# Optimization experiments

Measured on AMD Instinct MI355X. Metric: run time of the kernel, lower is better.

## Reference

```python
import jax, jax.numpy as jnp
import numpy as np

B = 8192
INPUT_DIM = 1024
PATH_DIM = 256
HIDDEN_DIM = 1024
OUTPUT_DIM = 1024
STEPS = 50


def setup_inputs() -> dict:
    key = jax.random.key(0)
    ks = jax.random.split(key, 12)
    s = lambda fan_in: 1.0 / np.sqrt(fan_in)
    x0 = jax.random.normal(ks[0], (B, INPUT_DIM), dtype=jnp.float32)
    W_pe = jax.random.uniform(ks[1], (INPUT_DIM, PATH_DIM), jnp.float32, -s(INPUT_DIM), s(INPUT_DIM))
    b_pe = jax.random.uniform(ks[2], (PATH_DIM,), jnp.float32, -s(INPUT_DIM), s(INPUT_DIM))
    W_hi = jax.random.uniform(ks[3], (INPUT_DIM, HIDDEN_DIM), jnp.float32, -s(INPUT_DIM), s(INPUT_DIM))
    b_hi = jax.random.uniform(ks[4], (HIDDEN_DIM,), jnp.float32, -s(INPUT_DIM), s(INPUT_DIM))
    f_in = HIDDEN_DIM + PATH_DIM
    W1 = jax.random.uniform(ks[5], (f_in, HIDDEN_DIM), jnp.float32, -s(f_in), s(f_in))
    b1 = jax.random.uniform(ks[6], (HIDDEN_DIM,), jnp.float32, -s(f_in), s(f_in))
    W2 = jax.random.uniform(ks[7], (HIDDEN_DIM, HIDDEN_DIM), jnp.float32, -s(HIDDEN_DIM), s(HIDDEN_DIM))
    b2 = jax.random.uniform(ks[8], (HIDDEN_DIM,), jnp.float32, -s(HIDDEN_DIM), s(HIDDEN_DIM))
    W_ro = jax.random.uniform(ks[9], (HIDDEN_DIM, OUTPUT_DIM), jnp.float32, -s(HIDDEN_DIM), s(HIDDEN_DIM))
    b_ro = jax.random.uniform(ks[10], (OUTPUT_DIM,), jnp.float32, -s(HIDDEN_DIM), s(HIDDEN_DIM))
    return {"x0": x0, "W_pe": W_pe, "b_pe": b_pe, "W_hi": W_hi, "b_hi": b_hi,
            "W1": W1, "b1": b1, "W2": W2, "b2": b2, "W_ro": W_ro, "b_ro": b_ro}


def reference(x0, W_pe, b_pe, W_hi, b_hi, W1, b1, W2, b2, W_ro, b_ro):
    dt = 1.0 / float(STEPS)
    g = x0 @ W_pe + b_pe          # [B, path_dim]
    z0 = x0 @ W_hi + b_hi          # [B, hidden_dim]
    ts = dt * jnp.arange(1, STEPS + 1, dtype=jnp.float32)  # t after each step

    def step(z, t):
        u_t = t * g                                  # [B, path_dim]
        inp = jnp.concatenate([z, u_t], axis=-1)     # [B, hidden+path]
        dz = jnp.tanh(inp @ W1 + b1) @ W2 + b2       # [B, hidden_dim]
        return z + dt * dz, None

    z, _ = jax.lax.scan(step, z0, ts)
    return z @ W_ro + b_ro
```

## Files before the change

kernel.cpp:

```cpp
#include <hip/hip_runtime.h>
#include <hip/hip_bf16.h>

typedef __hip_bfloat16 bf16;
typedef __bf16 bf16x8 __attribute__((ext_vector_type(8)));
typedef float f32x4 __attribute__((ext_vector_type(4)));

#define ROWS   32
#define HID    1024
#define PATH   256
#define NSTEP  50
#define P      1032
#define SMEM_BYTES (2 * ROWS * P * 2)

__device__ __forceinline__ f32x4 mfma16(bf16x8 a, bf16x8 b, f32x4 c) {
    return __builtin_amdgcn_mfma_f32_16x16x32_bf16(a, b, c, 0, 0, 0);
}

__device__ __forceinline__ float tanh_fast(float x) {
    float e = __expf(2.0f * x);
    return 1.0f - 2.0f / (e + 1.0f);
}

__device__ __forceinline__ bf16x8 ldcvt8(const float* __restrict__ p) {
    f32x4 lo = *(const f32x4*)p;
    f32x4 hi = *(const f32x4*)(p + 4);
    bf16x8 r;
    #pragma unroll
    for (int j = 0; j < 4; j++) { r[j] = (__bf16)lo[j]; r[4 + j] = (__bf16)hi[j]; }
    return r;
}

__global__ void pack_frag(const float* __restrict__ src, bf16* __restrict__ dst, int N) {
    int kb = blockIdx.x, nb = blockIdx.y, l = threadIdx.x;
    int lm = l & 15, lq = l >> 4;
    bf16x8 v;
    #pragma unroll
    for (int j = 0; j < 8; j++)
        v[j] = __float2bfloat16(src[(size_t)(kb * 32 + lq * 8 + j) * N + nb * 16 + lm]);
    *(bf16x8*)(dst + ((size_t)(kb * gridDim.y + nb) * 64 + l) * 8) = v;
}

template<int KB>
__device__ __forceinline__ void gemm4r(const bf16* __restrict__ lds,
                                       const bf16* __restrict__ Wp,
                                       int wave, int lane, int rot, f32x4 (&acc)[2][4]) {
    const int lm = lane & 15, lq = lane >> 4;
    #pragma unroll 2
    for (int kb = 0; kb < KB; kb++) {
        int kbr = kb + rot; if (kbr >= KB) kbr -= KB;
        const bf16* wp = Wp + (((size_t)kbr * 64 + wave * 4) * 64 + lane) * 8;
        bf16x8 w[4];
        #pragma unroll
        for (int nt = 0; nt < 4; nt++) w[nt] = *(const bf16x8*)(wp + nt * 512);
        bf16x8 a0 = *(const bf16x8*)(lds + lm * P + kbr * 32 + lq * 8);
        bf16x8 a1 = *(const bf16x8*)(lds + (16 + lm) * P + kbr * 32 + lq * 8);
        #pragma unroll
        for (int nt = 0; nt < 4; nt++) {
            acc[0][nt] = mfma16(a0, w[nt], acc[0][nt]);
            acc[1][nt] = mfma16(a1, w[nt], acc[1][nt]);
        }
    }
}

__global__ __launch_bounds__(1024) void cde_main(
    const float* __restrict__ x0,  const float* __restrict__ b_pe, const float* __restrict__ b_hi,
    const float* __restrict__ b1v, const float* __restrict__ b2v,  const float* __restrict__ b_ro,
    const bf16* __restrict__ WpeP, const bf16* __restrict__ WhiP,
    const bf16* __restrict__ W1zP, const bf16* __restrict__ W1uP,
    const bf16* __restrict__ W2P,  const bf16* __restrict__ WroP,
    float* __restrict__ out)
{
    extern __shared__ bf16 smem[];
    bf16* inp = smem;
    bf16* th  = smem + ROWS * P;

    const int tid  = threadIdx.x;
    const int wave = tid >> 6;
    const int lane = tid & 63;
    const int lm   = lane & 15;
    const int lq   = lane >> 4;
    const int rot  = (blockIdx.x >> 3) & 31;
    const long row0 = (long)blockIdx.x * ROWS;

    f32x4 z[2][4];
    f32x4 g[2];
    f32x4 c_u[2][4];

    #pragma unroll
    for (int nt = 0; nt < 4; nt++) {
        float b = b_hi[wave * 64 + nt * 16 + lm];
        #pragma unroll
        for (int r = 0; r < 4; r++) { z[0][nt][r] = b; z[1][nt][r] = b; }
    }
    {
        float b = b_pe[wave * 16 + lm];
        #pragma unroll
        for (int r = 0; r < 4; r++) { g[0][r] = b; g[1][r] = b; }
    }
    for (int kb = 0; kb < HID / 32; kb++) {
        int kbr = kb + rot; if (kbr >= 32) kbr -= 32;
        bf16x8 a0 = ldcvt8(x0 + (row0 +      lm) * HID + kbr * 32 + lq * 8);
        bf16x8 a1 = ldcvt8(x0 + (row0 + 16 + lm) * HID + kbr * 32 + lq * 8);
        const bf16* wp = WhiP + (((size_t)kbr * 64 + wave * 4) * 64 + lane) * 8;
        #pragma unroll
        for (int nt = 0; nt < 4; nt++) {
            bf16x8 bb = *(const bf16x8*)(wp + nt * 512);
            z[0][nt] = mfma16(a0, bb, z[0][nt]);
            z[1][nt] = mfma16(a1, bb, z[1][nt]);
        }
        bf16x8 pb = *(const bf16x8*)(WpeP + (((size_t)kbr * 16 + wave) * 64 + lane) * 8);
        g[0] = mfma16(a0, pb, g[0]);
        g[1] = mfma16(a1, pb, g[1]);
    }

    #pragma unroll
    for (int mt = 0; mt < 2; mt++)
        #pragma unroll
        for (int r = 0; r < 4; r++)
            inp[(mt * 16 + lq * 4 + r) * P + wave * 16 + lm] = __float2bfloat16(g[mt][r]);
    __syncthreads();
    #pragma unroll
    for (int mt = 0; mt < 2; mt++)
        #pragma unroll
        for (int nt = 0; nt < 4; nt++)
            #pragma unroll
            for (int r = 0; r < 4; r++) c_u[mt][nt][r] = 0.0f;
    for (int kb = 0; kb < PATH / 32; kb++) {
        const bf16* wp = W1uP + (((size_t)kb * 64 + wave * 4) * 64 + lane) * 8;
        bf16x8 a0 = *(const bf16x8*)(inp + lm * P + kb * 32 + lq * 8);
        bf16x8 a1 = *(const bf16x8*)(inp + (16 + lm) * P + kb * 32 + lq * 8);
        #pragma unroll
        for (int nt = 0; nt < 4; nt++) {
            bf16x8 bb = *(const bf16x8*)(wp + nt * 512);
            c_u[0][nt] = mfma16(a0, bb, c_u[0][nt]);
            c_u[1][nt] = mfma16(a1, bb, c_u[1][nt]);
        }
    }
    __syncthreads();

    float b1r[4], b2r[4];
    #pragma unroll
    for (int nt = 0; nt < 4; nt++) {
        b1r[nt] = b1v[wave * 64 + nt * 16 + lm];
        b2r[nt] = b2v[wave * 64 + nt * 16 + lm];
    }

    const float DT = 1.0f / (float)NSTEP;

    for (int s = 0; s < NSTEP; s++) {
        float t = DT * (float)(s + 1);

        #pragma unroll
        for (int mt = 0; mt < 2; mt++)
            #pragma unroll
            for (int nt = 0; nt < 4; nt++)
                #pragma unroll
                for (int r = 0; r < 4; r++)
                    inp[(mt * 16 + lq * 4 + r) * P + wave * 64 + nt * 16 + lm] =
                        __float2bfloat16(z[mt][nt][r]);
        __syncthreads();

        {
            f32x4 acc[2][4];
            #pragma unroll
            for (int mt = 0; mt < 2; mt++)
                #pragma unroll
                for (int nt = 0; nt < 4; nt++)
                    #pragma unroll
                    for (int r = 0; r < 4; r++)
                        acc[mt][nt][r] = fmaf(t, c_u[mt][nt][r], b1r[nt]);
            gemm4r<HID / 32>(inp, W1zP, wave, lane, rot, acc);
            #pragma unroll
            for (int mt = 0; mt < 2; mt++)
                #pragma unroll
                for (int nt = 0; nt < 4; nt++)
                    #pragma unroll
                    for (int r = 0; r < 4; r++)
                        th[(mt * 16 + lq * 4 + r) * P + wave * 64 + nt * 16 + lm] =
                            __float2bfloat16(tanh_fast(acc[mt][nt][r]));
        }
        __syncthreads();

        {
            f32x4 acc[2][4];
            #pragma unroll
            for (int nt = 0; nt < 4; nt++)
                #pragma unroll
                for (int r = 0; r < 4; r++) { acc[0][nt][r] = b2r[nt]; acc[1][nt][r] = b2r[nt]; }
            gemm4r<HID / 32>(th, W2P, wave, lane, rot, acc);
            #pragma unroll
            for (int mt = 0; mt < 2; mt++)
                #pragma unroll
                for (int nt = 0; nt < 4; nt++)
                    #pragma unroll
                    for (int r = 0; r < 4; r++)
                        z[mt][nt][r] += DT * acc[mt][nt][r];
        }
    }

    #pragma unroll
    for (int mt = 0; mt < 2; mt++)
        #pragma unroll
        for (int nt = 0; nt < 4; nt++)
            #pragma unroll
            for (int r = 0; r < 4; r++)
                inp[(mt * 16 + lq * 4 + r) * P + wave * 64 + nt * 16 + lm] =
                    __float2bfloat16(z[mt][nt][r]);
    __syncthreads();
    {
        f32x4 acc[2][4];
        #pragma unroll
        for (int nt = 0; nt < 4; nt++) {
            float b = b_ro[wave * 64 + nt * 16 + lm];
            #pragma unroll
            for (int r = 0; r < 4; r++) { acc[0][nt][r] = b; acc[1][nt][r] = b; }
        }
        gemm4r<HID / 32>(inp, WroP, wave, lane, rot, acc);
        #pragma unroll
        for (int mt = 0; mt < 2; mt++)
            #pragma unroll
            for (int nt = 0; nt < 4; nt++)
                #pragma unroll
                for (int r = 0; r < 4; r++)
                    out[(row0 + mt * 16 + lq * 4 + r) * HID + wave * 64 + nt * 16 + lm] =
                        acc[mt][nt][r];
    }
}

extern "C" void kernel_launch(void* const* d_in, const int* in_sizes, int n_in,
                              void* d_out, int out_size, void* d_ws, size_t ws_size,
                              hipStream_t stream) {
    (void)in_sizes; (void)n_in; (void)out_size; (void)ws_size;
    const float* x0  = (const float*)d_in[0];
    const float* Wpe = (const float*)d_in[1];
    const float* bpe = (const float*)d_in[2];
    const float* Whi = (const float*)d_in[3];
    const float* bhi = (const float*)d_in[4];
    const float* W1  = (const float*)d_in[5];
    const float* b1  = (const float*)d_in[6];
    const float* W2  = (const float*)d_in[7];
    const float* b2  = (const float*)d_in[8];
    const float* Wro = (const float*)d_in[9];
    const float* bro = (const float*)d_in[10];

    bf16* ws   = (bf16*)d_ws;
    bf16* WpeP = ws;
    bf16* WhiP = WpeP + 256 * 1024;
    bf16* W1zP = WhiP + 1024 * 1024;
    bf16* W1uP = W1zP + 1024 * 1024;
    bf16* W2P  = W1uP + 256 * 1024;
    bf16* WroP = W2P  + 1024 * 1024;

    hipLaunchKernelGGL(pack_frag, dim3(1024 / 32, 256 / 16), dim3(64), 0, stream, Wpe, WpeP, 256);
    hipLaunchKernelGGL(pack_frag, dim3(1024 / 32, 1024 / 16), dim3(64), 0, stream, Whi, WhiP, 1024);
    hipLaunchKernelGGL(pack_frag, dim3(1024 / 32, 1024 / 16), dim3(64), 0, stream, W1, W1zP, 1024);
    hipLaunchKernelGGL(pack_frag, dim3(256 / 32, 1024 / 16), dim3(64), 0, stream,
                       W1 + (size_t)1024 * 1024, W1uP, 1024);
    hipLaunchKernelGGL(pack_frag, dim3(1024 / 32, 1024 / 16), dim3(64), 0, stream, W2, W2P, 1024);
    hipLaunchKernelGGL(pack_frag, dim3(1024 / 32, 1024 / 16), dim3(64), 0, stream, Wro, WroP, 1024);

    hipFuncSetAttribute((const void*)cde_main,
                        hipFuncAttributeMaxDynamicSharedMemorySize, SMEM_BYTES);
    hipLaunchKernelGGL(cde_main, dim3(8192 / ROWS), dim3(1024), SMEM_BYTES, stream,
                       x0, bpe, bhi, b1, b2, bro, WpeP, WhiP, W1zP, W1uP, W2P, WroP,
                       (float*)d_out);
}
```

Measured before the change: 3.145 ms.

## Remap waves to one row tile by eight column tiles per wave

Changes the per-wave output tile from two 16-row tiles by four 16-column tiles to a single 16-row tile by eight column tiles, across all GEMMs in the kernel. Each wave now reads one LDS A-fragment per k-block instead of two, but loads twice as many weight fragments from global memory, and each weight fragment is now fetched by two waves. Weight loads are split into two batches of four to bound register use.

```diff
diff --git a/kernel.cpp b/kernel.cpp
--- a/kernel.cpp
+++ b/kernel.cpp
@@ -41,24 +41,25 @@
 }
 
 template<int KB>
-__device__ __forceinline__ void gemm4r(const bf16* __restrict__ lds,
+__device__ __forceinline__ void gemm8p(const bf16* __restrict__ lds,
                                        const bf16* __restrict__ Wp,
-                                       int wave, int lane, int rot, f32x4 (&acc)[2][4]) {
+                                       int cg, int mt, int lane, int rot,
+                                       f32x4 (&acc)[8]) {
     const int lm = lane & 15, lq = lane >> 4;
     #pragma unroll 2
     for (int kb = 0; kb < KB; kb++) {
         int kbr = kb + rot; if (kbr >= KB) kbr -= KB;
-        const bf16* wp = Wp + (((size_t)kbr * 64 + wave * 4) * 64 + lane) * 8;
+        const bf16* wp = Wp + (((size_t)kbr * 64 + cg * 8) * 64 + lane) * 8;
+        bf16x8 a = *(const bf16x8*)(lds + (mt * 16 + lm) * P + kbr * 32 + lq * 8);
         bf16x8 w[4];
         #pragma unroll
         for (int nt = 0; nt < 4; nt++) w[nt] = *(const bf16x8*)(wp + nt * 512);
-        bf16x8 a0 = *(const bf16x8*)(lds + lm * P + kbr * 32 + lq * 8);
-        bf16x8 a1 = *(const bf16x8*)(lds + (16 + lm) * P + kbr * 32 + lq * 8);
-        #pragma unroll
-        for (int nt = 0; nt < 4; nt++) {
-            acc[0][nt] = mfma16(a0, w[nt], acc[0][nt]);
-            acc[1][nt] = mfma16(a1, w[nt], acc[1][nt]);
-        }
+        #pragma unroll
+        for (int nt = 0; nt < 4; nt++) acc[nt] = mfma16(a, w[nt], acc[nt]);
+        #pragma unroll
+        for (int nt = 0; nt < 4; nt++) w[nt] = *(const bf16x8*)(wp + (4 + nt) * 512);
+        #pragma unroll
+        for (int nt = 0; nt < 4; nt++) acc[4 + nt] = mfma16(a, w[nt], acc[4 + nt]);
     }
 }
 
@@ -79,70 +80,70 @@
     const int lane = tid & 63;
     const int lm   = lane & 15;
     const int lq   = lane >> 4;
+    const int mt   = wave >> 3;
+    const int cg   = wave & 7;
     const int rot  = (blockIdx.x >> 3) & 31;
     const long row0 = (long)blockIdx.x * ROWS;
 
-    f32x4 z[2][4];
+    f32x4 z[8];
+    f32x4 c_u[8];
     f32x4 g[2];
-    f32x4 c_u[2][4];
-
-    #pragma unroll
-    for (int nt = 0; nt < 4; nt++) {
-        float b = b_hi[wave * 64 + nt * 16 + lm];
-        #pragma unroll
-        for (int r = 0; r < 4; r++) { z[0][nt][r] = b; z[1][nt][r] = b; }
-    }
-    {
-        float b = b_pe[wave * 16 + lm];
-        #pragma unroll
-        for (int r = 0; r < 4; r++) { g[0][r] = b; g[1][r] = b; }
+
+    #pragma unroll
+    for (int nt = 0; nt < 8; nt++) {
+        float b = b_hi[cg * 128 + nt * 16 + lm];
+        #pragma unroll
+        for (int r = 0; r < 4; r++) z[nt][r] = b;
+    }
+    #pragma unroll
+    for (int nt = 0; nt < 2; nt++) {
+        float b = b_pe[cg * 32 + nt * 16 + lm];
+        #pragma unroll
+        for (int r = 0; r < 4; r++) g[nt][r] = b;
     }
     for (int kb = 0; kb < HID / 32; kb++) {
         int kbr = kb + rot; if (kbr >= 32) kbr -= 32;
-        bf16x8 a0 = ldcvt8(x0 + (row0 +      lm) * HID + kbr * 32 + lq * 8);
-        bf16x8 a1 = ldcvt8(x0 + (row0 + 16 + lm) * HID + kbr * 32 + lq * 8);
-        const bf16* wp = WhiP + (((size_t)kbr * 64 + wave * 4) * 64 + lane) * 8;
-        #pragma unroll
-        for (int nt = 0; nt < 4; nt++) {
+        bf16x8 a = ldcvt8(x0 + (row0 + mt * 16 + lm) * HID + kbr * 32 + lq * 8);
+        const bf16* wp = WhiP + (((size_t)kbr * 64 + cg * 8) * 64 + lane) * 8;
+        #pragma unroll
+        for (int nt = 0; nt < 8; nt++) {
             bf16x8 bb = *(const bf16x8*)(wp + nt * 512);
-            z[0][nt] = mfma16(a0, bb, z[0][nt]);
-            z[1][nt] = mfma16(a1, bb, z[1][nt]);
-        }
-        bf16x8 pb = *(const bf16x8*)(WpeP + (((size_t)kbr * 16 + wave) * 64 + lane) * 8);
-        g[0] = mfma16(a0, pb, g[0]);
-        g[1] = mfma16(a1, pb, g[1]);
-    }
-
-    #pragma unroll
-    for (int mt = 0; mt < 2; mt++)
+            z[nt] = mfma16(a, bb, z[nt]);
+        }
+        const bf16* pp = WpeP + (((size_t)kbr * 16 + cg * 2) * 64 + lane) * 8;
+        #pragma unroll
+        for (int nt = 0; nt < 2; nt++) {
+            bf16x8 bb = *(const bf16x8*)(pp + nt * 512);
+            g[nt] = mfma16(a, bb, g[nt]);
+        }
+    }
+
+    #pragma unroll
+    for (int nt = 0; nt < 2; nt++)
         #pragma unroll
         for (int r = 0; r < 4; r++)
-            inp[(mt * 16 + lq * 4 + r) * P + wave * 16 + lm] = __float2bfloat16(g[mt][r]);
+            inp[(mt * 16 + lq * 4 + r) * P + cg * 32 + nt * 16 + lm] = __float2bfloat16(g[nt][r]);
     __syncthreads();
     #pragma unroll
-    for (int mt = 0; mt < 2; mt++)
-        #pragma unroll
-        for (int nt = 0; nt < 4; nt++)
-            #pragma unroll
-            for (int r = 0; r < 4; r++) c_u[mt][nt][r] = 0.0f;
+    for (int nt = 0; nt < 8; nt++)
+        #pragma unroll
+        for (int r = 0; r < 4; r++) c_u[nt][r] = 0.0f;
     for (int kb = 0; kb < PATH / 32; kb++) {
-        const bf16* wp = W1uP + (((size_t)kb * 64 + wave * 4) * 64 + lane) * 8;
-        bf16x8 a0 = *(const bf16x8*)(inp + lm * P + kb * 32 + lq * 8);
-        bf16x8 a1 = *(const bf16x8*)(inp + (16 + lm) * P + kb * 32 + lq * 8);
-        #pragma unroll
-        for (int nt = 0; nt < 4; nt++) {
+        const bf16* wp = W1uP + (((size_t)kb * 64 + cg * 8) * 64 + lane) * 8;
+        bf16x8 a = *(const bf16x8*)(inp + (mt * 16 + lm) * P + kb * 32 + lq * 8);
+        #pragma unroll
+        for (int nt = 0; nt < 8; nt++) {
             bf16x8 bb = *(const bf16x8*)(wp + nt * 512);
-            c_u[0][nt] = mfma16(a0, bb, c_u[0][nt]);
-            c_u[1][nt] = mfma16(a1, bb, c_u[1][nt]);
+            c_u[nt] = mfma16(a, bb, c_u[nt]);
         }
     }
     __syncthreads();
 
-    float b1r[4], b2r[4];
-    #pragma unroll
-    for (int nt = 0; nt < 4; nt++) {
-        b1r[nt] = b1v[wave * 64 + nt * 16 + lm];
-        b2r[nt] = b2v[wave * 64 + nt * 16 + lm];
+    float b1r[8], b2r[8];
+    #pragma unroll
+    for (int nt = 0; nt < 8; nt++) {
+        b1r[nt] = b1v[cg * 128 + nt * 16 + lm];
+        b2r[nt] = b2v[cg * 128 + nt * 16 + lm];
     }
 
     const float DT = 1.0f / (float)NSTEP;
@@ -151,79 +152,67 @@
         float t = DT * (float)(s + 1);
 
         #pragma unroll
-        for (int mt = 0; mt < 2; mt++)
-            #pragma unroll
-            for (int nt = 0; nt < 4; nt++)
+        for (int nt = 0; nt < 8; nt++)
+            #pragma unroll
+            for (int r = 0; r < 4; r++)
+                inp[(mt * 16 + lq * 4 + r) * P + cg * 128 + nt * 16 + lm] =
+                    __float2bfloat16(z[nt][r]);
+        __syncthreads();
+
+        {
+            f32x4 acc[8];
+            #pragma unroll
+            for (int nt = 0; nt < 8; nt++)
                 #pragma unroll
                 for (int r = 0; r < 4; r++)
-                    inp[(mt * 16 + lq * 4 + r) * P + wave * 64 + nt * 16 + lm] =
-                        __float2bfloat16(z[mt][nt][r]);
+                    acc[nt][r] = fmaf(t, c_u[nt][r], b1r[nt]);
+            gemm8p<HID / 32>(inp, W1zP, cg, mt, lane, rot, acc);
+            #pragma unroll
+            for (int nt = 0; nt < 8; nt++)
+                #pragma unroll
+                for (int r = 0; r < 4; r++)
+                    th[(mt * 16 + lq * 4 + r) * P + cg * 128 + nt * 16 + lm] =
+                        __float2bfloat16(tanh_fast(acc[nt][r]));
+        }
         __syncthreads();
 
         {
-            f32x4 acc[2][4];
-            #pragma unroll
-            for (int mt = 0; mt < 2; mt++)
-                #pragma unroll
-                for (int nt = 0; nt < 4; nt++)
-                    #pragma unroll
-                    for (int r = 0; r < 4; r++)
-                        acc[mt][nt][r] = fmaf(t, c_u[mt][nt][r], b1r[nt]);
-            gemm4r<HID / 32>(inp, W1zP, wave, lane, rot, acc);
-            #pragma unroll
-            for (int mt = 0; mt < 2; mt++)
-                #pragma unroll
-                for (int nt = 0; nt < 4; nt++)
-                    #pragma unroll
-                    for (int r = 0; r < 4; r++)
-                        th[(mt * 16 + lq * 4 + r) * P + wave * 64 + nt * 16 + lm] =
-                            __float2bfloat16(tanh_fast(acc[mt][nt][r]));
-        }
-        __syncthreads();
-
-        {
-            f32x4 acc[2][4];
-            #pragma unroll
-            for (int nt = 0; nt < 4; nt++)
-                #pragma unroll
-                for (int r = 0; r < 4; r++) { acc[0][nt][r] = b2r[nt]; acc[1][nt][r] = b2r[nt]; }
-            gemm4r<HID / 32>(th, W2P, wave, lane, rot, acc);
-            #pragma unroll
-            for (int mt = 0; mt < 2; mt++)
-                #pragma unroll
-                for (int nt = 0; nt < 4; nt++)
-                    #pragma unroll
-                    for (int r = 0; r < 4; r++)
-                        z[mt][nt][r] += DT * acc[mt][nt][r];
-        }
-    }
-
-    #pragma unroll
-    for (int mt = 0; mt < 2; mt++)
-        #pragma unroll
-        for (int nt = 0; nt < 4; nt++)
-            #pragma unroll
-            for (int r = 0; r < 4; r++)
-                inp[(mt * 16 + lq * 4 + r) * P + wave * 64 + nt * 16 + lm] =
-                    __float2bfloat16(z[mt][nt][r]);
+            f32x4 acc[8];
+            #pragma unroll
+            for (int nt = 0; nt < 8; nt++)
+                #pragma unroll
+                for (int r = 0; r < 4; r++) acc[nt][r] = b2r[nt];
+            gemm8p<HID / 32>(th, W2P, cg, mt, lane, rot, acc);
+            #pragma unroll
+            for (int nt = 0; nt < 8; nt++)
+                #pragma unroll
+                for (int r = 0; r < 4; r++)
+                    z[nt][r] += DT * acc[nt][r];
+        }
+    }
+
+    #pragma unroll
+    for (int nt = 0; nt < 8; nt++)
+        #pragma unroll
+        for (int r = 0; r < 4; r++)
+            inp[(mt * 16 + lq * 4 + r) * P + cg * 128 + nt * 16 + lm] =
+                __float2bfloat16(z[nt][r]);
     __syncthreads();
     {
-        f32x4 acc[2][4];
-        #pragma unroll
-        for (int nt = 0; nt < 4; nt++) {
-            float b = b_ro[wave * 64 + nt * 16 + lm];
-            #pragma unroll
-            for (int r = 0; r < 4; r++) { acc[0][nt][r] = b; acc[1][nt][r] = b; }
-        }
-        gemm4r<HID / 32>(inp, WroP, wave, lane, rot, acc);
-        #pragma unroll
-        for (int mt = 0; mt < 2; mt++)
-            #pragma unroll
-            for (int nt = 0; nt < 4; nt++)
-                #pragma unroll
-                for (int r = 0; r < 4; r++)
-                    out[(row0 + mt * 16 + lq * 4 + r) * HID + wave * 64 + nt * 16 + lm] =
-                        acc[mt][nt][r];
+        f32x4 acc[8];
+        #pragma unroll
+        for (int nt = 0; nt < 8; nt++) {
+            float b = b_ro[cg * 128 + nt * 16 + lm];
+            #pragma unroll
+            for (int r = 0; r < 4; r++) acc[nt][r] = b;
+        }
+        gemm8p<HID / 32>(inp, WroP, cg, mt, lane, rot, acc);
+        #pragma unroll
+        for (int nt = 0; nt < 8; nt++)
+            #pragma unroll
+            for (int r = 0; r < 4; r++)
+                out[(row0 + mt * 16 + lq * 4 + r) * HID + cg * 128 + nt * 16 + lm] =
+                    acc[nt][r];
     }
 }
 
```

Result: slower. 3.835 ms (+21.9%).
